# Performance work log

Measured on AMD Instinct MI355X. Metric: run time of the kernel, lower is better.

The kernel has to match this reference:

```python
import jax, jax.numpy as jnp
import numpy as np

N = 50000
E = 600000
D_IN = 128
D_HID = 128
D_OUT = 40
BN_EPS = 1e-5


def setup_inputs() -> dict:
    key = jax.random.key(0)
    ks = jax.random.split(key, 16)
    g = lambda k, *s: (jax.random.normal(k, s, jnp.float32) * 0.05)
    return {
        "x": jax.random.normal(ks[0], (N, D_IN), jnp.float32),
        "edge_index": jax.random.randint(ks[1], (2, E), 0, N, dtype=jnp.int64),
        "W0": g(ks[2], D_IN, D_HID), "b0": jnp.zeros((D_HID,), jnp.float32),
        "W1": g(ks[3], D_HID, D_HID), "b1": jnp.zeros((D_HID,), jnp.float32),
        "W2": g(ks[4], D_HID, D_OUT), "b2": jnp.zeros((D_OUT,), jnp.float32),
        "g0": 1.0 + g(ks[5], D_HID), "be0": g(ks[6], D_HID),
        "m0": g(ks[7], D_HID), "v0": 0.5 + jax.random.uniform(ks[8], (D_HID,), jnp.float32),
        "g1": 1.0 + g(ks[9], D_HID), "be1": g(ks[10], D_HID),
        "m1": g(ks[11], D_HID), "v1": 0.5 + jax.random.uniform(ks[12], (D_HID,), jnp.float32),
    }


def reference(x, edge_index, W0, b0, W1, b1, W2, b2,
              g0, be0, m0, v0, g1, be1, m1, v1):
    n = x.shape[0]
    loop = jnp.arange(n, dtype=edge_index.dtype)
    # GCN with self-loops: A_hat = A + I, symmetric normalization
    src = jnp.concatenate([edge_index[0], loop])
    dst = jnp.concatenate([edge_index[1], loop])
    deg = jax.ops.segment_sum(jnp.ones_like(dst, jnp.float32), dst, num_segments=n)
    dinv = jax.lax.rsqrt(jnp.maximum(deg, 1.0))
    norm = dinv[src] * dinv[dst]  # [E+N]

    def conv(h, W, b):
        h = h @ W + b                                   # [N, d_out]
        msg = norm[:, None] * h[src]                    # gather + scale
        return jax.ops.segment_sum(msg, dst, num_segments=n)

    def bn_relu(h, g, be, m, v):
        return jax.nn.relu((h - m) * (g * jax.lax.rsqrt(v + BN_EPS)) + be)

    h = bn_relu(conv(x, W0, b0), g0, be0, m0, v0)
    h = bn_relu(conv(h, W1, b1), g1, be1, m1, v1)
    h = conv(h, W2, b2)
    return jax.nn.log_softmax(h, axis=-1)
```

## Files before the change

kernel.cpp:

```cpp
#include <hip/hip_runtime.h>
#include <math.h>

#define BN_EPS 1e-5f
#define CAP 96

typedef unsigned short ushort_t;
typedef __attribute__((ext_vector_type(8))) short short8;
typedef __attribute__((ext_vector_type(4))) float floatx4;

__device__ inline ushort_t f2b(float f) {
    unsigned u = __float_as_uint(f);
    unsigned r = u + 0x7FFFu + ((u >> 16) & 1u);
    return (ushort_t)(r >> 16);
}
__device__ inline float b2f(ushort_t b) { return __uint_as_float(((unsigned)b) << 16); }
__device__ inline float2 u2f2(unsigned u) {
    return make_float2(b2f((ushort_t)(u & 0xffffu)), b2f((ushort_t)(u >> 16)));
}

__device__ inline void cast_weights(const float* __restrict__ W0, const float* __restrict__ W1,
                                    const float* __restrict__ W2, ushort_t* __restrict__ Wt0,
                                    ushort_t* __restrict__ Wt1, ushort_t* __restrict__ Wt2,
                                    int i) {
    if (i < 16384) {
        int nn = i >> 7, k = i & 127;
        Wt0[i] = f2b(W0[k * 128 + nn]);
    } else if (i < 32768) {
        int j = i - 16384;
        int nn = j >> 7, k = j & 127;
        Wt1[j] = f2b(W1[k * 128 + nn]);
    } else if (i < 40960) {
        int j = i - 32768;
        int nn = j >> 7, k = j & 127;
        Wt2[j] = (nn < 40) ? f2b(W2[k * 40 + nn]) : (ushort_t)0;
    }
}

__global__ __launch_bounds__(256) void k_fill_cast(
    const int* __restrict__ ei, int* __restrict__ cnt, ushort_t* __restrict__ ell,
    const float* __restrict__ W0, const float* __restrict__ W1, const float* __restrict__ W2,
    ushort_t* __restrict__ Wt0, ushort_t* __restrict__ Wt1, ushort_t* __restrict__ Wt2,
    int E, int FB)
{
    int bid = blockIdx.x;
    if (bid < FB) {
        int e = bid * 256 + threadIdx.x;
        if (e < E) {
            int s = ei[e];
            int d = ei[E + e];
            int p = atomicAdd(&cnt[d], 1);
            if (p < CAP) ell[(size_t)d * CAP + p] = (ushort_t)s;
        }
        return;
    }
    cast_weights(W0, W1, W2, Wt0, Wt1, Wt2, (bid - FB) * 256 + threadIdx.x);
}

template<int NT, bool AF32>
__global__ __launch_bounds__(256) void k_gemm(const void* __restrict__ Av,
                                              const ushort_t* __restrict__ Wt,
                                              const float* __restrict__ bias,
                                              const int* __restrict__ cnt,
                                              ushort_t* __restrict__ C,
                                              int M, int ncols) {
    __shared__ ushort_t Ws[NT * 128];
    const int tid = threadIdx.x;
    const int ntiles = (M + 127) >> 7;
    const int wave = tid >> 6, lane = tid & 63;
    const int m = lane & 15, quad = lane >> 4;
    constexpr int CT = NT / 16;
    const int r0 = wave * 32;

    for (int t = blockIdx.x; t < ntiles; t += gridDim.x) {
        const int rbase = t << 7;
#pragma unroll
        for (int p = 0; p < NT / 16; ++p) {
            int cid = p * 256 + tid;
            int nr = cid >> 4, seg = cid & 15;
            *(uint4*)(Ws + nr * 128 + ((seg ^ (nr & 15)) << 3)) =
                *(const uint4*)(Wt + (size_t)cid * 8);
        }
        __syncthreads();

        floatx4 acc[2][CT];
#pragma unroll
        for (int rt = 0; rt < 2; ++rt)
#pragma unroll
            for (int ct = 0; ct < CT; ++ct) acc[rt][ct] = (floatx4){0.f, 0.f, 0.f, 0.f};

        const int ra = rbase + r0 + m;
        const int rb = ra + 16;
        const bool oka = ra < M, okb = rb < M;

#pragma unroll
        for (int ks = 0; ks < 4; ++ks) {
            int ko = ks * 32 + quad * 8;
            short8 a0 = {0, 0, 0, 0, 0, 0, 0, 0}, a1 = a0;
            if (AF32) {
                const float* A32 = (const float*)Av;
                if (oka) {
                    const float* p = A32 + (size_t)ra * 128 + ko;
                    float4 f0 = *(const float4*)p, f1 = *(const float4*)(p + 4);
                    a0[0] = f2b(f0.x); a0[1] = f2b(f0.y); a0[2] = f2b(f0.z); a0[3] = f2b(f0.w);
                    a0[4] = f2b(f1.x); a0[5] = f2b(f1.y); a0[6] = f2b(f1.z); a0[7] = f2b(f1.w);
                }
                if (okb) {
                    const float* p = A32 + (size_t)rb * 128 + ko;
                    float4 f0 = *(const float4*)p, f1 = *(const float4*)(p + 4);
                    a1[0] = f2b(f0.x); a1[1] = f2b(f0.y); a1[2] = f2b(f0.z); a1[3] = f2b(f0.w);
                    a1[4] = f2b(f1.x); a1[5] = f2b(f1.y); a1[6] = f2b(f1.z); a1[7] = f2b(f1.w);
                }
            } else {
                const ushort_t* A16 = (const ushort_t*)Av;
                if (oka) a0 = *(const short8*)(A16 + (size_t)ra * 128 + ko);
                if (okb) a1 = *(const short8*)(A16 + (size_t)rb * 128 + ko);
            }
#pragma unroll
            for (int ct = 0; ct < CT; ++ct) {
                short8 b = *(const short8*)(Ws + (ct * 16 + m) * 128 + (((ks * 4 + quad) ^ m) << 3));
                acc[0][ct] = __builtin_amdgcn_mfma_f32_16x16x32_bf16(a0, b, acc[0][ct], 0, 0, 0);
                acc[1][ct] = __builtin_amdgcn_mfma_f32_16x16x32_bf16(a1, b, acc[1][ct], 0, 0, 0);
            }
        }

        float dsc[2][4];
#pragma unroll
        for (int rt = 0; rt < 2; ++rt)
#pragma unroll
            for (int r = 0; r < 4; ++r) {
                int gr = rbase + r0 + rt * 16 + quad * 4 + r;
                dsc[rt][r] = (gr < M) ? rsqrtf((float)(cnt[gr] + 1)) : 0.f;
            }

        __syncthreads();
        constexpr int SEGN = NT / 8, CMASK = SEGN - 1;
#pragma unroll
        for (int rt = 0; rt < 2; ++rt)
#pragma unroll
            for (int ct = 0; ct < CT; ++ct) {
                int col = ct * 16 + m;
                float bv = (col < ncols) ? bias[col] : 0.f;
                int seg = col >> 3, cl = col & 7;
#pragma unroll
                for (int r = 0; r < 4; ++r) {
                    int row = r0 + rt * 16 + quad * 4 + r;
                    Ws[row * NT + ((seg ^ (row & CMASK)) << 3) + cl] =
                        f2b((acc[rt][ct][r] + bv) * dsc[rt][r]);
                }
            }
        __syncthreads();
        constexpr int CPT = (128 * SEGN) / 256;
#pragma unroll
        for (int p = 0; p < CPT; ++p) {
            int cid = p * 256 + tid;
            int row = cid / SEGN, seg = cid & CMASK;
            int gr = rbase + row;
            if (gr < M)
                *(uint4*)(C + (size_t)gr * NT + seg * 8) =
                    *(const uint4*)(Ws + row * NT + ((seg ^ (row & CMASK)) << 3));
        }
        __syncthreads();
    }
}

template<int NT>
__global__ __launch_bounds__(256) void fused_ag(
    const ushort_t* __restrict__ h,
    const int* __restrict__ cnt,
    const ushort_t* __restrict__ ell,
    const float* __restrict__ g, const float* __restrict__ be,
    const float* __restrict__ mB, const float* __restrict__ v,
    const ushort_t* __restrict__ Wt,
    const float* __restrict__ bias,
    ushort_t* __restrict__ C,
    int M, int ncols)
{
    __shared__ ushort_t As[64 * 128];
    __shared__ ushort_t Ws[NT * 128];
    const int tid = threadIdx.x;
    const int ntiles = (M + 63) >> 6;
    const int wave = tid >> 6, lane = tid & 63;
    const int m = lane & 15, quad = lane >> 4;
    constexpr int CT = NT / 16;
    const int r0 = wave * 16;
    const unsigned* h2 = (const unsigned*)h;
    unsigned* As2 = (unsigned*)As;

    const int c0 = lane * 2;
    const float s0f = g[c0] * rsqrtf(v[c0] + BN_EPS);
    const float s1f = g[c0 + 1] * rsqrtf(v[c0 + 1] + BN_EPS);
    const float m0v = mB[c0], m1v = mB[c0 + 1], b0v = be[c0], b1v = be[c0 + 1];

    for (int t = blockIdx.x; t < ntiles; t += gridDim.x) {
        const int rbase = t << 6;

#pragma unroll
        for (int p = 0; p < NT / 16; ++p) {
            int cid = p * 256 + tid;
            int nr = cid >> 4, seg = cid & 15;
            *(uint4*)(Ws + nr * 128 + ((seg ^ (nr & 15)) << 3)) =
                *(const uint4*)(Wt + (size_t)cid * 8);
        }

        for (int rr = 0; rr < 16; ++rr) {
            const int rl = r0 + rr;
            const int gr = rbase + rl;
            unsigned ov = 0;
            if (gr < M) {
                int cd = cnt[gr];
                float dv = rsqrtf((float)(cd + 1));
                float2 hv = u2f2(h2[(size_t)gr * 64 + lane]);
                float ax = hv.x, ay = hv.y;
                int c = min(cd, CAP);
                const uint4* rowv = (const uint4*)(ell + (size_t)gr * CAP);
                int k = 0;
                for (; k + 8 <= c; k += 8) {
                    uint4 iv = rowv[k >> 3];
                    int s[8] = {(int)(iv.x & 0xffffu), (int)(iv.x >> 16),
                                (int)(iv.y & 0xffffu), (int)(iv.y >> 16),
                                (int)(iv.z & 0xffffu), (int)(iv.z >> 16),
                                (int)(iv.w & 0xffffu), (int)(iv.w >> 16)};
#pragma unroll
                    for (int j = 0; j < 8; ++j) {
                        float2 tt = u2f2(h2[(size_t)s[j] * 64 + lane]);
                        ax += tt.x;
                        ay += tt.y;
                    }
                }
                if (k < c) {
                    int rem = c - k;
                    uint4 iv = rowv[k >> 3];
                    int sr[8] = {(int)(iv.x & 0xffffu), (int)(iv.x >> 16),
                                 (int)(iv.y & 0xffffu), (int)(iv.y >> 16),
                                 (int)(iv.z & 0xffffu), (int)(iv.z >> 16),
                                 (int)(iv.w & 0xffffu), (int)(iv.w >> 16)};
                    int s[8];
#pragma unroll
                    for (int j = 0; j < 8; ++j) s[j] = (j < rem) ? sr[j] : 0;
#pragma unroll
                    for (int j = 0; j < 8; ++j) {
                        float2 tt = u2f2(h2[(size_t)s[j] * 64 + lane]);
                        ax += (j < rem) ? tt.x : 0.f;
                        ay += (j < rem) ? tt.y : 0.f;
                    }
                }
                ax *= dv;
                ay *= dv;
                float o0 = fmaxf(fmaf(ax - m0v, s0f, b0v), 0.f);
                float o1 = fmaxf(fmaf(ay - m1v, s1f, b1v), 0.f);
                ov = (unsigned)f2b(o0) | ((unsigned)f2b(o1) << 16);
            }
            As2[rl * 64 + (((lane >> 2) ^ (rl & 15)) << 2) + (lane & 3)] = ov;
        }
        __syncthreads();

        floatx4 acc[CT];
#pragma unroll
        for (int ct = 0; ct < CT; ++ct) acc[ct] = (floatx4){0.f, 0.f, 0.f, 0.f};
#pragma unroll
        for (int ks = 0; ks < 4; ++ks) {
            short8 a0 = *(const short8*)(As + (r0 + m) * 128 + (((ks * 4 + quad) ^ m) << 3));
#pragma unroll
            for (int ct = 0; ct < CT; ++ct) {
                short8 b = *(const short8*)(Ws + (ct * 16 + m) * 128 + (((ks * 4 + quad) ^ m) << 3));
                acc[ct] = __builtin_amdgcn_mfma_f32_16x16x32_bf16(a0, b, acc[ct], 0, 0, 0);
            }
        }

        float dsc[4];
#pragma unroll
        for (int r = 0; r < 4; ++r) {
            int gr2 = rbase + r0 + quad * 4 + r;
            dsc[r] = (gr2 < M) ? rsqrtf((float)(cnt[gr2] + 1)) : 0.f;
        }

        __syncthreads();
        constexpr int SEGN = NT / 8, CMASK = SEGN - 1;
#pragma unroll
        for (int ct = 0; ct < CT; ++ct) {
            int col = ct * 16 + m;
            float bv = (col < ncols) ? bias[col] : 0.f;
            int seg = col >> 3, cl = col & 7;
#pragma unroll
            for (int r = 0; r < 4; ++r) {
                int row = r0 + quad * 4 + r;
                As[row * NT + ((seg ^ (row & CMASK)) << 3) + cl] =
                    f2b((acc[ct][r] + bv) * dsc[r]);
            }
        }
        __syncthreads();
        constexpr int CPT = (64 * SEGN) / 256;
#pragma unroll
        for (int p = 0; p < CPT; ++p) {
            int cid = p * 256 + tid;
            int row = cid / SEGN, seg = cid & CMASK;
            int gr = rbase + row;
            if (gr < M)
                *(uint4*)(C + (size_t)gr * NT + seg * 8) =
                    *(const uint4*)(As + row * NT + ((seg ^ (row & CMASK)) << 3));
        }
        __syncthreads();
    }
}

__global__ __launch_bounds__(256) void k_agg40(const ushort_t* __restrict__ h,
                                               const int* __restrict__ cnt,
                                               const ushort_t* __restrict__ ell,
                                               float* __restrict__ out, int n) {
    int wv = __builtin_amdgcn_readfirstlane((blockIdx.x * 256 + threadIdx.x) >> 6);
    int lane = threadIdx.x & 63;
    if (wv >= n) return;
    int cd = cnt[wv];
    float dv = rsqrtf((float)(cd + 1));
    float acc = b2f(h[(size_t)wv * 64 + lane]);
    int c = min(cd, CAP);
    const ushort_t* row = ell + (size_t)wv * CAP;
    int k = 0;
    for (; k + 8 <= c; k += 8) {
        int s[8];
#pragma unroll
        for (int j = 0; j < 8; ++j) s[j] = row[k + j];
#pragma unroll
        for (int j = 0; j < 8; ++j) acc += b2f(h[(size_t)s[j] * 64 + lane]);
    }
    if (k < c) {
        int rem = c - k;
        int s[8];
#pragma unroll
        for (int j = 0; j < 8; ++j) {
            int sr = row[k + j];
            s[j] = (j < rem) ? sr : 0;
        }
#pragma unroll
        for (int j = 0; j < 8; ++j) {
            float t = b2f(h[(size_t)s[j] * 64 + lane]);
            acc += (j < rem) ? t : 0.f;
        }
    }
    acc *= dv;
    bool act = lane < 40;
    float xv = act ? acc : -INFINITY;
    float mx = xv;
#pragma unroll
    for (int off = 32; off > 0; off >>= 1) mx = fmaxf(mx, __shfl_xor(mx, off, 64));
    float ex = act ? expf(acc - mx) : 0.f;
    float se = ex;
#pragma unroll
    for (int off = 32; off > 0; off >>= 1) se += __shfl_xor(se, off, 64);
    float r = acc - mx - logf(se);
    if (act) out[(size_t)wv * 40 + lane] = r;
}


extern "C" void kernel_launch(void* const* d_in, const int* in_sizes, int n_in,
                              void* d_out, int out_size, void* d_ws, size_t ws_size,
                              hipStream_t stream) {
    const float* x = (const float*)d_in[0];
    const int* ei = (const int*)d_in[1];
    const float* W0 = (const float*)d_in[2];
    const float* b0 = (const float*)d_in[3];
    const float* W1 = (const float*)d_in[4];
    const float* b1 = (const float*)d_in[5];
    const float* W2 = (const float*)d_in[6];
    const float* b2 = (const float*)d_in[7];
    const float* g0 = (const float*)d_in[8];
    const float* be0 = (const float*)d_in[9];
    const float* m0 = (const float*)d_in[10];
    const float* v0 = (const float*)d_in[11];
    const float* g1 = (const float*)d_in[12];
    const float* be1 = (const float*)d_in[13];
    const float* m1 = (const float*)d_in[14];
    const float* v1 = (const float*)d_in[15];
    float* out = (float*)d_out;

    const int N = in_sizes[0] / 128;
    const int E = in_sizes[1] / 2;

    char* wp = (char*)d_ws;
    auto alloc = [&](size_t bytes) -> char* {
        char* p = wp;
        wp += (bytes + 255) & ~(size_t)255;
        return p;
    };
    int* cnt = (int*)alloc((size_t)N * 4);
    ushort_t* ell = (ushort_t*)alloc(((size_t)N * CAP + 16) * 2);
    ushort_t* hA = (ushort_t*)alloc((size_t)N * 128 * 2);
    ushort_t* hA2 = (ushort_t*)alloc((size_t)N * 128 * 2);
    ushort_t* hL = (ushort_t*)alloc((size_t)N * 64 * 2);
    ushort_t* Wt0 = (ushort_t*)alloc(128 * 128 * 2);
    ushort_t* Wt1 = (ushort_t*)alloc(128 * 128 * 2);
    ushort_t* Wt2 = (ushort_t*)alloc(64 * 128 * 2);

    const int GB = (N + 127) / 128;
    const int TG = (N + 63) / 64;
    const int FB = (E + 255) / 256;
    const int CB = 160;

    hipMemsetAsync(cnt, 0, (size_t)N * 4, stream);
    k_fill_cast<<<FB + CB, 256, 0, stream>>>(ei, cnt, ell, W0, W1, W2,
                                             Wt0, Wt1, Wt2, E, FB);
    k_gemm<128, true><<<GB, 256, 0, stream>>>(x, Wt0, b0, cnt, hA, N, 128);
    fused_ag<128><<<TG, 256, 0, stream>>>(hA, cnt, ell, g0, be0, m0, v0,
                                          Wt1, b1, hA2, N, 128);
    fused_ag<64><<<TG, 256, 0, stream>>>(hA2, cnt, ell, g1, be1, m1, v1,
                                         Wt2, b2, hL, N, 40);
    k_agg40<<<(N + 3) / 4, 256, 0, stream>>>(hL, cnt, ell, out, N);
}
```

Before: 277.4 us.

## Shrink fused aggregate-GEMM tile to 16 rows with 512-thread blocks

```diff
diff --git a/kernel.cpp b/kernel.cpp
--- a/kernel.cpp
+++ b/kernel.cpp
@@ -164,7 +164,7 @@
 }
 
 template<int NT>
-__global__ __launch_bounds__(256) void fused_ag(
+__global__ __launch_bounds__(512) void fused_ag(
     const ushort_t* __restrict__ h,
     const int* __restrict__ cnt,
     const ushort_t* __restrict__ ell,
@@ -175,14 +175,13 @@
     ushort_t* __restrict__ C,
     int M, int ncols)
 {
-    __shared__ ushort_t As[64 * 128];
+    __shared__ ushort_t As[16 * 128];
     __shared__ ushort_t Ws[NT * 128];
     const int tid = threadIdx.x;
-    const int ntiles = (M + 63) >> 6;
+    const int ntiles = (M + 15) >> 4;
     const int wave = tid >> 6, lane = tid & 63;
     const int m = lane & 15, quad = lane >> 4;
     constexpr int CT = NT / 16;
-    const int r0 = wave * 16;
     const unsigned* h2 = (const unsigned*)h;
     unsigned* As2 = (unsigned*)As;
 
@@ -192,18 +191,17 @@
     const float m0v = mB[c0], m1v = mB[c0 + 1], b0v = be[c0], b1v = be[c0 + 1];
 
     for (int t = blockIdx.x; t < ntiles; t += gridDim.x) {
-        const int rbase = t << 6;
-
-#pragma unroll
-        for (int p = 0; p < NT / 16; ++p) {
-            int cid = p * 256 + tid;
+        const int rbase = t << 4;
+
+        for (int cid = tid; cid < NT * 16; cid += 512) {
             int nr = cid >> 4, seg = cid & 15;
             *(uint4*)(Ws + nr * 128 + ((seg ^ (nr & 15)) << 3)) =
                 *(const uint4*)(Wt + (size_t)cid * 8);
         }
 
-        for (int rr = 0; rr < 16; ++rr) {
-            const int rl = r0 + rr;
+#pragma unroll
+        for (int rr = 0; rr < 2; ++rr) {
+            const int rl = wave * 2 + rr;
             const int gr = rbase + rl;
             unsigned ov = 0;
             if (gr < M) {
@@ -250,49 +248,42 @@
                 float o1 = fmaxf(fmaf(ay - m1v, s1f, b1v), 0.f);
                 ov = (unsigned)f2b(o0) | ((unsigned)f2b(o1) << 16);
             }
-            As2[rl * 64 + (((lane >> 2) ^ (rl & 15)) << 2) + (lane & 3)] = ov;
-        }
-        __syncthreads();
-
-        floatx4 acc[CT];
-#pragma unroll
-        for (int ct = 0; ct < CT; ++ct) acc[ct] = (floatx4){0.f, 0.f, 0.f, 0.f};
-#pragma unroll
-        for (int ks = 0; ks < 4; ++ks) {
-            short8 a0 = *(const short8*)(As + (r0 + m) * 128 + (((ks * 4 + quad) ^ m) << 3));
-#pragma unroll
-            for (int ct = 0; ct < CT; ++ct) {
-                short8 b = *(const short8*)(Ws + (ct * 16 + m) * 128 + (((ks * 4 + quad) ^ m) << 3));
-                acc[ct] = __builtin_amdgcn_mfma_f32_16x16x32_bf16(a0, b, acc[ct], 0, 0, 0);
+            As2[rl * 64 + (((lane >> 2) ^ rl) << 2) + (lane & 3)] = ov;
+        }
+        __syncthreads();
+
+        floatx4 acc = (floatx4){0.f, 0.f, 0.f, 0.f};
+        if (wave < CT) {
+#pragma unroll
+            for (int ks = 0; ks < 4; ++ks) {
+                short8 a0 = *(const short8*)(As + m * 128 + (((ks * 4 + quad) ^ m) << 3));
+                short8 b = *(const short8*)(Ws + (wave * 16 + m) * 128 + (((ks * 4 + quad) ^ m) << 3));
+                acc = __builtin_amdgcn_mfma_f32_16x16x32_bf16(a0, b, acc, 0, 0, 0);
             }
         }
 
         float dsc[4];
 #pragma unroll
         for (int r = 0; r < 4; ++r) {
-            int gr2 = rbase + r0 + quad * 4 + r;
+            int gr2 = rbase + quad * 4 + r;
             dsc[r] = (gr2 < M) ? rsqrtf((float)(cnt[gr2] + 1)) : 0.f;
         }
 
         __syncthreads();
         constexpr int SEGN = NT / 8, CMASK = SEGN - 1;
-#pragma unroll
-        for (int ct = 0; ct < CT; ++ct) {
-            int col = ct * 16 + m;
+        if (wave < CT) {
+            int col = wave * 16 + m;
             float bv = (col < ncols) ? bias[col] : 0.f;
             int seg = col >> 3, cl = col & 7;
 #pragma unroll
             for (int r = 0; r < 4; ++r) {
-                int row = r0 + quad * 4 + r;
+                int row = quad * 4 + r;
                 As[row * NT + ((seg ^ (row & CMASK)) << 3) + cl] =
-                    f2b((acc[ct][r] + bv) * dsc[r]);
-            }
-        }
-        __syncthreads();
-        constexpr int CPT = (64 * SEGN) / 256;
-#pragma unroll
-        for (int p = 0; p < CPT; ++p) {
-            int cid = p * 256 + tid;
+                    f2b((acc[r] + bv) * dsc[r]);
+            }
+        }
+        __syncthreads();
+        for (int cid = tid; cid < 16 * SEGN; cid += 512) {
             int row = cid / SEGN, seg = cid & CMASK;
             int gr = rbase + row;
             if (gr < M)
@@ -392,7 +383,7 @@
     ushort_t* Wt2 = (ushort_t*)alloc(64 * 128 * 2);
 
     const int GB = (N + 127) / 128;
-    const int TG = (N + 63) / 64;
+    const int TG = (N + 15) / 16;
     const int FB = (E + 255) / 256;
     const int CB = 160;
 
@@ -400,9 +391,9 @@
     k_fill_cast<<<FB + CB, 256, 0, stream>>>(ei, cnt, ell, W0, W1, W2,
                                              Wt0, Wt1, Wt2, E, FB);
     k_gemm<128, true><<<GB, 256, 0, stream>>>(x, Wt0, b0, cnt, hA, N, 128);
-    fused_ag<128><<<TG, 256, 0, stream>>>(hA, cnt, ell, g0, be0, m0, v0,
+    fused_ag<128><<<TG, 512, 0, stream>>>(hA, cnt, ell, g0, be0, m0, v0,
                                           Wt1, b1, hA2, N, 128);
-    fused_ag<64><<<TG, 256, 0, stream>>>(hA2, cnt, ell, g1, be1, m1, v1,
+    fused_ag<64><<<TG, 512, 0, stream>>>(hA2, cnt, ell, g1, be1, m1, v1,
                                          Wt2, b2, hL, N, 40);
     k_agg40<<<(N + 3) / 4, 256, 0, stream>>>(hL, cnt, ell, out, N);
 }
```

Result: faster. 235.8 us (-15.0%).
